# Performance work log

Hardware: AMD Instinct MI355X
Metric: run time of the kernel (lower is better)

## Reference

```python
import jax, jax.numpy as jnp
import numpy as np

N = 100000       # num nodes
E = 1000000      # num edges
D_IN = 128       # input feature dim
D_H = 64         # hidden = output dim
EPS = 1e-5       # GraphNorm eps
SLOPE = 0.2      # LeakyReLU negative slope


def _glorot(key, shape):
    lim = float(np.sqrt(6.0 / (shape[0] + shape[1])))
    return jax.random.uniform(key, shape, jnp.float32, -lim, lim)


def setup_inputs() -> dict:
    key = jax.random.key(0)
    ks = jax.random.split(key, 6)
    return {
        "x": jax.random.normal(ks[0], (N, D_IN), jnp.float32),
        "edge_index": jax.random.randint(ks[1], (2, E), 0, N),
        "W_in": _glorot(ks[2], (D_IN, D_H)),
        "b_in": jnp.zeros((D_H,), jnp.float32),
        "W1": _glorot(ks[3], (D_H, D_H)),
        "b1": jnp.zeros((D_H,), jnp.float32),
        "gn1_alpha": jnp.ones((D_H,), jnp.float32),
        "gn1_gamma": jnp.ones((D_H,), jnp.float32),
        "gn1_beta": jnp.zeros((D_H,), jnp.float32),
        "W2": _glorot(ks[4], (D_H, D_H)),
        "b2": jnp.zeros((D_H,), jnp.float32),
        "gn2_alpha": jnp.ones((D_H,), jnp.float32),
        "gn2_gamma": jnp.ones((D_H,), jnp.float32),
        "gn2_beta": jnp.zeros((D_H,), jnp.float32),
    }


def gcn_conv(x, W, b, src, dst):
    # GCNConv with added self-loops and symmetric normalization:
    # out = D^{-1/2} (A + I) D^{-1/2} (x W) + b
    xw = x @ W                                                 # [N, D]
    ones = jnp.ones((src.shape[0],), x.dtype)
    deg = jax.ops.segment_sum(ones, dst, num_segments=x.shape[0]) + 1.0  # +1 self-loop
    dinv = jax.lax.rsqrt(deg)                                  # [N]
    coef = dinv[src] * dinv[dst]                               # [E]
    agg = jax.ops.segment_sum(xw[src] * coef[:, None], dst, num_segments=x.shape[0])
    return agg + xw * (dinv * dinv)[:, None] + b


def graph_norm(x, alpha, gamma, beta):
    # PyG GraphNorm over a single graph: per-feature mean/var over all nodes
    mean = jnp.mean(x, axis=0)
    c = x - alpha * mean
    var = jnp.mean(c * c, axis=0)
    return gamma * c * jax.lax.rsqrt(var + EPS) + beta


def reference(x, edge_index, W_in, b_in, W1, b1, gn1_alpha, gn1_gamma, gn1_beta,
              W2, b2, gn2_alpha, gn2_gamma, gn2_beta):
    src, dst = edge_index[0], edge_index[1]
    h = x @ W_in + b_in                                        # input projection
    h = graph_norm(gcn_conv(h, W1, b1, src, dst), gn1_alpha, gn1_gamma, gn1_beta)
    h = jnp.where(h > 0, h, SLOPE * h)                         # LeakyReLU(0.2); dropout=eval (identity)
    h = graph_norm(gcn_conv(h, W2, b2, src, dst), gn2_alpha, gn2_gamma, gn2_beta)
    return h                                                    # [N, D_H]
```

## Files before the change

kernel.cpp:

```cpp
#include <hip/hip_runtime.h>
#include <stdint.h>

#define N_NODES 100000
#define N_EDGES 1000000
#define D_IN 128
#define D_H 64
#define EPS 1e-5f
#define SLOPE 0.2f

typedef unsigned short u16;
typedef unsigned int u32;
typedef __attribute__((ext_vector_type(8))) short bf16x8;
typedef __attribute__((ext_vector_type(4))) float f32x4;

#define SLAB_U16 ((size_t)(N_NODES + 1) * 16)
#define SLAB_D32 ((size_t)(N_NODES + 1) * 8)

__device__ __forceinline__ float bf2f(u16 u) {
    union { u32 i; float f; } v; v.i = ((u32)u) << 16; return v.f;
}
__device__ __forceinline__ u16 f2bf(float f) {
    union { float f; u32 i; } v; v.f = f;
    u32 r = (v.i + 0x7fffu + ((v.i >> 16) & 1u)) >> 16;
    return (u16)r;
}
__device__ __forceinline__ bool is_f32(const void* flagp) {
    return *(const u32*)flagp == 0x3F800000u;
}
__device__ __forceinline__ float loadf(const void* p, size_t i, bool m) {
    return m ? ((const float*)p)[i] : bf2f(((const u16*)p)[i]);
}

__global__ void kprep(const void* __restrict__ W_in, const void* __restrict__ b_in,
                      const void* __restrict__ W1, const void* __restrict__ W2,
                      const void* __restrict__ flagp,
                      u16* __restrict__ WcT, u16* __restrict__ W2T,
                      float* __restrict__ bc, u16* __restrict__ xwb_pad)
{
    bool m = is_f32(flagp);
    int t = threadIdx.x;
    if (blockIdx.x < 64) {
        int c = blockIdx.x;
        __shared__ float w1c[D_H];
        if (t < D_H) w1c[t] = loadf(W1, t * D_H + c, m);
        __syncthreads();
        float acc = 0.f;
        #pragma unroll 8
        for (int j = 0; j < D_H; j++) acc += loadf(W_in, t * D_H + j, m) * w1c[j];
        WcT[c * D_IN + t] = f2bf(acc);
        if (t == 0) {
            float b = 0.f;
            for (int j = 0; j < D_H; j++) b += loadf(b_in, j, m) * w1c[j];
            bc[c] = b;
        }
        if (c == 0 && t < D_H) {
            int s = t >> 4, w = t & 15;
            xwb_pad[(size_t)s * SLAB_U16 + (size_t)N_NODES * 16 + w] = 0;
        }
    } else {
        int idx = (blockIdx.x - 64) * 128 + t;
        int n = idx >> 6, k = idx & 63;
        W2T[n * D_H + k] = f2bf(loadf(W2, k * D_H + n, m));
    }
}

__global__ void kfill(const int* __restrict__ ei, int* __restrict__ cnt,
                      int* __restrict__ bucket)
{
    int e = blockIdx.x * blockDim.x + threadIdx.x;
    if (e >= N_EDGES) return;
    int s = ei[e];
    int d = ei[N_EDGES + e];
    int slot = atomicAdd(&cnt[d], 1);
    if (slot < 64) bucket[(size_t)d * 64 + slot] = s;
}

__global__ __launch_bounds__(256) void kgemm1(const void* __restrict__ x,
        const u16* __restrict__ WcT, const float* __restrict__ bc,
        const int* __restrict__ cnt, const void* __restrict__ flagp,
        u16* __restrict__ xwb)
{
    bool m = is_f32(flagp);
    __shared__ __align__(16) u16 xs[64 * 136];
    __shared__ __align__(16) u16 WT[64 * 136];
    int tid = threadIdx.x;
    int row0 = blockIdx.x * 64;
    for (int i = tid; i < 64 * 32; i += 256) {
        int r = i >> 5, kq = (i & 31) * 4;
        *(ushort4*)(WT + r * 136 + kq) = *(const ushort4*)(WcT + r * D_IN + kq);
    }
    for (int i = tid; i < 64 * 32; i += 256) {
        int r = i >> 5, kq = (i & 31) * 4;
        int gr = row0 + r;
        ushort4 u = make_ushort4(0, 0, 0, 0);
        if (gr < N_NODES) {
            if (m) {
                float4 v = *(const float4*)((const float*)x + (size_t)gr * D_IN + kq);
                u = make_ushort4(f2bf(v.x), f2bf(v.y), f2bf(v.z), f2bf(v.w));
            } else {
                u = *(const ushort4*)((const u16*)x + (size_t)gr * D_IN + kq);
            }
        }
        *(ushort4*)(xs + r * 136 + kq) = u;
    }
    __syncthreads();
    int w = tid >> 6, L = tid & 63;
    int q = L >> 4, c = L & 15;
    f32x4 acc[4];
    #pragma unroll
    for (int ct = 0; ct < 4; ct++) {
        float b = bc[ct * 16 + c];
        acc[ct] = (f32x4){b, b, b, b};
    }
    const u16* ap = xs + (w * 16 + c) * 136 + q * 8;
    #pragma unroll
    for (int kk = 0; kk < 4; kk++) {
        bf16x8 af = *(const bf16x8*)(ap + kk * 32);
        #pragma unroll
        for (int ct = 0; ct < 4; ct++) {
            bf16x8 bfr = *(const bf16x8*)(WT + (ct * 16 + c) * 136 + kk * 32 + q * 8);
            acc[ct] = __builtin_amdgcn_mfma_f32_16x16x32_bf16(af, bfr, acc[ct], 0, 0, 0);
        }
    }
    #pragma unroll
    for (int r = 0; r < 4; r++) {
        int gr = row0 + w * 16 + q * 4 + r;
        if (gr < N_NODES) {
            float ds = rsqrtf((float)cnt[gr] + 1.0f);
            #pragma unroll
            for (int ct = 0; ct < 4; ct++)
                xwb[(size_t)ct * SLAB_U16 + (size_t)gr * 16 + c] = f2bf(acc[ct][r] * ds);
        }
    }
}

__global__ __launch_bounds__(256) void kagg(const u16* __restrict__ xwb,
        const int* __restrict__ cnt, const int* __restrict__ bucket,
        const void* __restrict__ bvec, const void* __restrict__ flagp,
        u16* __restrict__ ybuf, float* __restrict__ accum)
{
    bool m = is_f32(flagp);
    __shared__ float red_s[4][64], red_q[4][64];
    int tid = threadIdx.x;
    int wv = tid >> 6, L = tid & 63;
    int r = L >> 3, c = L & 7;
    int node0 = blockIdx.x * 32 + wv * 8;

    int cnt8 = cnt[node0 + (L & 7)];
    int tl = L >> 4, sl = L & 15;
    int raw0 = bucket[(size_t)(node0 + tl) * 64 + sl];
    int raw1 = bucket[(size_t)(node0 + 4 + tl) * 64 + sl];

    int sv[16];
    #pragma unroll
    for (int n = 0; n < 8; n++) {
        int dgn = min(__shfl(cnt8, n), 64);
        int ngl = node0 + n;
        #pragma unroll
        for (int g = 0; g < 2; g++) {
            int slot = g * 8 + r;
            int rw = __shfl((n < 4) ? raw0 : raw1, (n & 3) * 16 + slot);
            sv[n * 2 + g] = slot < dgn ? rw : (slot == dgn ? ngl : N_NODES);
        }
    }

    int cvr = __shfl(cnt8, r);
    int dgr = min(cvr, 64);
    int nr = node0 + r;
    float dd = rsqrtf((float)cvr + 1.0f);
    bool anyrem = __any(dgr >= 16);

    #pragma unroll
    for (int p = 0; p < 4; p++) {
        const u32* slab = (const u32*)xwb + (size_t)p * SLAB_D32;
        u32 q[16];
        #pragma unroll
        for (int i = 0; i < 16; i++) q[i] = slab[(size_t)sv[i] * 8 + c];

        float fA0 = 0.f, fA1 = 0.f;
        #pragma unroll
        for (int n = 0; n < 8; n++) {
            u32 a = q[n * 2], b = q[n * 2 + 1];
            float f0 = __uint_as_float(a << 16) + __uint_as_float(b << 16);
            float f1 = __uint_as_float(a & 0xffff0000u) + __uint_as_float(b & 0xffff0000u);
            f0 += __shfl_xor(f0, 8);  f1 += __shfl_xor(f1, 8);
            f0 += __shfl_xor(f0, 16); f1 += __shfl_xor(f1, 16);
            f0 += __shfl_xor(f0, 32); f1 += __shfl_xor(f1, 32);
            if (r == n) { fA0 = f0; fA1 = f1; }
        }

        if (anyrem) {
            for (int s = 16; s <= 64; s++) {
                if (!__any(s <= dgr)) break;
                if (s <= dgr) {
                    int sv2 = (s < dgr) ? bucket[(size_t)nr * 64 + s] : nr;
                    u32 v = slab[(size_t)sv2 * 8 + c];
                    fA0 += __uint_as_float(v << 16);
                    fA1 += __uint_as_float(v & 0xffff0000u);
                }
            }
        }

        float b0 = loadf(bvec, p * 16 + 2 * c, m);
        float b1 = loadf(bvec, p * 16 + 2 * c + 1, m);
        float y0 = dd * fA0 + b0;
        float y1 = dd * fA1 + b1;
        ((u32*)ybuf)[(size_t)p * SLAB_D32 + (size_t)nr * 8 + c] =
            (u32)f2bf(y0) | ((u32)f2bf(y1) << 16);

        float s0 = y0, s1 = y1, q0 = y0 * y0, q1 = y1 * y1;
        s0 += __shfl_xor(s0, 8);  s1 += __shfl_xor(s1, 8);
        q0 += __shfl_xor(q0, 8);  q1 += __shfl_xor(q1, 8);
        s0 += __shfl_xor(s0, 16); s1 += __shfl_xor(s1, 16);
        q0 += __shfl_xor(q0, 16); q1 += __shfl_xor(q1, 16);
        s0 += __shfl_xor(s0, 32); s1 += __shfl_xor(s1, 32);
        q0 += __shfl_xor(q0, 32); q1 += __shfl_xor(q1, 32);
        if (r == 0) {
            red_s[wv][p * 16 + 2 * c] = s0;  red_s[wv][p * 16 + 2 * c + 1] = s1;
            red_q[wv][p * 16 + 2 * c] = q0;  red_q[wv][p * 16 + 2 * c + 1] = q1;
        }
    }

    __syncthreads();
    if (tid < 64) {
        atomicAdd(&accum[tid],      red_s[0][tid] + red_s[1][tid] + red_s[2][tid] + red_s[3][tid]);
        atomicAdd(&accum[64 + tid], red_q[0][tid] + red_q[1][tid] + red_q[2][tid] + red_q[3][tid]);
    }
}

__global__ __launch_bounds__(256) void kgemm2(const u16* __restrict__ y1b,
        const u16* __restrict__ W2T, const float* __restrict__ accum,
        const void* __restrict__ alpha, const void* __restrict__ gamma,
        const void* __restrict__ beta, const void* __restrict__ flagp,
        const int* __restrict__ cnt, u16* __restrict__ xwb)
{
    bool m = is_f32(flagp);
    __shared__ __align__(16) u16 hs[64 * 72];
    __shared__ __align__(16) u16 WT[64 * 72];
    __shared__ float aL[64], cL[64];
    int tid = threadIdx.x;
    if (tid < 64) {
        float mean = accum[tid] * (1.0f / N_NODES);
        float al = loadf(alpha, tid, m);
        float var = accum[64 + tid] * (1.0f / N_NODES) - mean * mean * al * (2.0f - al);
        var = fmaxf(var, 0.f);
        float a = loadf(gamma, tid, m) * rsqrtf(var + EPS);
        aL[tid] = a;
        cL[tid] = loadf(beta, tid, m) - a * al * mean;
    }
    for (int i = tid; i < 64 * 16; i += 256) {
        int r = i >> 4, kq = (i & 15) * 4;
        *(ushort4*)(WT + r * 72 + kq) = *(const ushort4*)(W2T + r * D_H + kq);
    }
    __syncthreads();
    int row0 = blockIdx.x * 64;
    for (int i = tid; i < 64 * 16; i += 256) {
        int r = i >> 4, kq = (i & 15) * 4;
        int gr = row0 + r;
        ushort4 u = make_ushort4(0, 0, 0, 0);
        if (gr < N_NODES) {
            int s = kq >> 4, off = kq & 15;
            u = *(const ushort4*)(y1b + (size_t)s * SLAB_U16 + (size_t)gr * 16 + off);
        }
        float h0 = aL[kq + 0] * bf2f(u.x) + cL[kq + 0]; h0 = h0 > 0.f ? h0 : SLOPE * h0;
        float h1 = aL[kq + 1] * bf2f(u.y) + cL[kq + 1]; h1 = h1 > 0.f ? h1 : SLOPE * h1;
        float h2 = aL[kq + 2] * bf2f(u.z) + cL[kq + 2]; h2 = h2 > 0.f ? h2 : SLOPE * h2;
        float h3 = aL[kq + 3] * bf2f(u.w) + cL[kq + 3]; h3 = h3 > 0.f ? h3 : SLOPE * h3;
        *(ushort4*)(hs + r * 72 + kq) = make_ushort4(f2bf(h0), f2bf(h1), f2bf(h2), f2bf(h3));
    }
    __syncthreads();
    int w = tid >> 6, L = tid & 63;
    int q = L >> 4, c = L & 15;
    f32x4 acc[4] = {};
    const u16* ap = hs + (w * 16 + c) * 72 + q * 8;
    #pragma unroll
    for (int kk = 0; kk < 2; kk++) {
        bf16x8 af = *(const bf16x8*)(ap + kk * 32);
        #pragma unroll
        for (int ct = 0; ct < 4; ct++) {
            bf16x8 bfr = *(const bf16x8*)(WT + (ct * 16 + c) * 72 + kk * 32 + q * 8);
            acc[ct] = __builtin_amdgcn_mfma_f32_16x16x32_bf16(af, bfr, acc[ct], 0, 0, 0);
        }
    }
    #pragma unroll
    for (int r = 0; r < 4; r++) {
        int gr = row0 + w * 16 + q * 4 + r;
        if (gr < N_NODES) {
            float ds = rsqrtf((float)cnt[gr] + 1.0f);
            #pragma unroll
            for (int ct = 0; ct < 4; ct++)
                xwb[(size_t)ct * SLAB_U16 + (size_t)gr * 16 + c] = f2bf(acc[ct][r] * ds);
        }
    }
}

__global__ __launch_bounds__(256) void kout(const u16* __restrict__ y2b,
        const float* __restrict__ accum2, const void* __restrict__ alpha,
        const void* __restrict__ gamma, const void* __restrict__ beta,
        const void* __restrict__ flagp, void* __restrict__ out)
{
    bool m = is_f32(flagp);
    __shared__ float a2[64], c2[64];
    int tid = threadIdx.x;
    if (tid < 64) {
        float mean = accum2[tid] * (1.0f / N_NODES);
        float al = loadf(alpha, tid, m);
        float var = accum2[64 + tid] * (1.0f / N_NODES) - mean * mean * al * (2.0f - al);
        var = fmaxf(var, 0.f);
        float a = loadf(gamma, tid, m) * rsqrtf(var + EPS);
        a2[tid] = a;
        c2[tid] = loadf(beta, tid, m) - a * al * mean;
    }
    __syncthreads();
    int gid = blockIdx.x * 256 + tid;
    int nd = gid >> 4, q4 = gid & 15;
    int s = q4 >> 2, pr = q4 & 3;
    const u32* yp = (const u32*)y2b + (size_t)s * SLAB_D32 + (size_t)nd * 8 + pr * 2;
    u32 v0 = yp[0];
    u32 v1 = yp[1];
    int f = q4 * 4;
    float o0 = a2[f + 0] * __uint_as_float(v0 << 16)          + c2[f + 0];
    float o1 = a2[f + 1] * __uint_as_float(v0 & 0xffff0000u)  + c2[f + 1];
    float o2 = a2[f + 2] * __uint_as_float(v1 << 16)          + c2[f + 2];
    float o3 = a2[f + 3] * __uint_as_float(v1 & 0xffff0000u)  + c2[f + 3];
    if (m) {
        *(float4*)((float*)out + (size_t)nd * 64 + f) = make_float4(o0, o1, o2, o3);
    } else {
        u32 p0 = (u32)f2bf(o0) | ((u32)f2bf(o1) << 16);
        u32 p1 = (u32)f2bf(o2) | ((u32)f2bf(o3) << 16);
        *(uint2*)((u32*)out + (size_t)nd * 32 + f / 2) = make_uint2(p0, p1);
    }
}

extern "C" void kernel_launch(void* const* d_in, const int* in_sizes, int n_in,
                              void* d_out, int out_size, void* d_ws, size_t ws_size,
                              hipStream_t stream)
{
    const void* x    = d_in[0];
    const int*  ei   = (const int*)d_in[1];
    const void* W_in = d_in[2];
    const void* b_in = d_in[3];
    const void* W1   = d_in[4];
    const void* b1   = d_in[5];
    const void* gn1a = d_in[6];
    const void* gn1g = d_in[7];
    const void* gn1b = d_in[8];
    const void* W2   = d_in[9];
    const void* b2   = d_in[10];
    const void* gn2a = d_in[11];
    const void* gn2g = d_in[12];
    const void* gn2b = d_in[13];

    char* ws = (char*)d_ws;
    int*   cnt    = (int*)(ws + 0);
    float* accum  = (float*)(ws + 400000);
    float* bc     = (float*)(ws + 402048);
    u16*   WcT    = (u16*)(ws + 402432);
    u16*   W2T    = (u16*)(ws + 418816);
    int*   bucket = (int*)(ws + 1235200);
    u16*   bufA   = (u16*)(ws + 26835200);
    u16*   bufB   = (u16*)(ws + 39635456);

    hipMemsetAsync(ws, 0, 400000 + 1024, stream);

    kprep<<<96, 128, 0, stream>>>(W_in, b_in, W1, W2, gn1a, WcT, W2T, bc, bufA);
    kfill<<<(N_EDGES + 255) / 256, 256, 0, stream>>>(ei, cnt, bucket);
    kgemm1<<<(N_NODES + 63) / 64, 256, 0, stream>>>(x, WcT, bc, cnt, gn1a, bufA);
    kagg<<<N_NODES / 32, 256, 0, stream>>>(bufA, cnt, bucket, b1, gn1a, bufB, accum);
    kgemm2<<<(N_NODES + 63) / 64, 256, 0, stream>>>(bufB, W2T, accum, gn1a, gn1g, gn1b, gn1a, cnt, bufA);
    kagg<<<N_NODES / 32, 256, 0, stream>>>(bufA, cnt, bucket, b2, gn1a, bufB, accum + 128);
    kout<<<N_NODES * 16 / 256, 256, 0, stream>>>(bufB, accum + 128, gn2a, gn2g, gn2b, gn1a, d_out);
}
```

Baseline: 413.8 us.

## Split aggregation into per-slab passes and fuse weight prep with edge bucketing

The aggregation kernel is split into four launches, one per 16-feature slab. Each pass gathers only a 3.2 MB slab, so the random neighbor gathers can hit in L2/MALL instead of streaming across all slabs in one kernel. The weight-prep and edge-bucket fill kernels are merged into one launch, and bucket writes use nontemporal stores. The cost is re-reading the bucket and count arrays and recomputing indices in every pass, plus more kernel launches.

```diff
diff --git a/kernel.cpp b/kernel.cpp
--- a/kernel.cpp
+++ b/kernel.cpp
@@ -31,23 +31,28 @@
     return m ? ((const float*)p)[i] : bf2f(((const u16*)p)[i]);
 }
 
-__global__ void kprep(const void* __restrict__ W_in, const void* __restrict__ b_in,
-                      const void* __restrict__ W1, const void* __restrict__ W2,
-                      const void* __restrict__ flagp,
-                      u16* __restrict__ WcT, u16* __restrict__ W2T,
-                      float* __restrict__ bc, u16* __restrict__ xwb_pad)
+__global__ __launch_bounds__(256) void kpf(const void* __restrict__ W_in,
+                     const void* __restrict__ b_in,
+                     const void* __restrict__ W1, const void* __restrict__ W2,
+                     const void* __restrict__ flagp, const int* __restrict__ ei,
+                     u16* __restrict__ WcT, u16* __restrict__ W2T,
+                     float* __restrict__ bc, u16* __restrict__ xwb_pad,
+                     int* __restrict__ cnt, int* __restrict__ bucket)
 {
     bool m = is_f32(flagp);
     int t = threadIdx.x;
-    if (blockIdx.x < 64) {
-        int c = blockIdx.x;
+    int bid = blockIdx.x;
+    if (bid < 64) {
+        int c = bid;
         __shared__ float w1c[D_H];
         if (t < D_H) w1c[t] = loadf(W1, t * D_H + c, m);
         __syncthreads();
-        float acc = 0.f;
-        #pragma unroll 8
-        for (int j = 0; j < D_H; j++) acc += loadf(W_in, t * D_H + j, m) * w1c[j];
-        WcT[c * D_IN + t] = f2bf(acc);
+        if (t < D_IN) {
+            float acc = 0.f;
+            #pragma unroll 8
+            for (int j = 0; j < D_H; j++) acc += loadf(W_in, t * D_H + j, m) * w1c[j];
+            WcT[c * D_IN + t] = f2bf(acc);
+        }
         if (t == 0) {
             float b = 0.f;
             for (int j = 0; j < D_H; j++) b += loadf(b_in, j, m) * w1c[j];
@@ -57,22 +62,20 @@
             int s = t >> 4, w = t & 15;
             xwb_pad[(size_t)s * SLAB_U16 + (size_t)N_NODES * 16 + w] = 0;
         }
-    } else {
-        int idx = (blockIdx.x - 64) * 128 + t;
+    } else if (bid < 80) {
+        int idx = (bid - 64) * 256 + t;
         int n = idx >> 6, k = idx & 63;
         W2T[n * D_H + k] = f2bf(loadf(W2, k * D_H + n, m));
-    }
-}
-
-__global__ void kfill(const int* __restrict__ ei, int* __restrict__ cnt,
-                      int* __restrict__ bucket)
-{
-    int e = blockIdx.x * blockDim.x + threadIdx.x;
-    if (e >= N_EDGES) return;
-    int s = ei[e];
-    int d = ei[N_EDGES + e];
-    int slot = atomicAdd(&cnt[d], 1);
-    if (slot < 64) bucket[(size_t)d * 64 + slot] = s;
+    } else {
+        int e = (bid - 80) * 256 + t;
+        if (e < N_EDGES) {
+            int s = ei[e];
+            int d = ei[N_EDGES + e];
+            int slot = atomicAdd(&cnt[d], 1);
+            if (slot < 64)
+                __builtin_nontemporal_store(s, &bucket[(size_t)d * 64 + slot]);
+        }
+    }
 }
 
 __global__ __launch_bounds__(256) void kgemm1(const void* __restrict__ x,
@@ -134,13 +137,13 @@
     }
 }
 
-__global__ __launch_bounds__(256) void kagg(const u16* __restrict__ xwb,
+__global__ __launch_bounds__(256) void kagg_pass(const u16* __restrict__ xwb,
         const int* __restrict__ cnt, const int* __restrict__ bucket,
         const void* __restrict__ bvec, const void* __restrict__ flagp,
-        u16* __restrict__ ybuf, float* __restrict__ accum)
-{
-    bool m = is_f32(flagp);
-    __shared__ float red_s[4][64], red_q[4][64];
+        u16* __restrict__ ybuf, float* __restrict__ accum, int pass)
+{
+    bool m = is_f32(flagp);
+    __shared__ float red_s[4][16], red_q[4][16];
     int tid = threadIdx.x;
     int wv = tid >> 6, L = tid & 63;
     int r = L >> 3, c = L & 7;
@@ -170,61 +173,59 @@
     float dd = rsqrtf((float)cvr + 1.0f);
     bool anyrem = __any(dgr >= 16);
 
-    #pragma unroll
-    for (int p = 0; p < 4; p++) {
-        const u32* slab = (const u32*)xwb + (size_t)p * SLAB_D32;
-        u32 q[16];
-        #pragma unroll
-        for (int i = 0; i < 16; i++) q[i] = slab[(size_t)sv[i] * 8 + c];
-
-        float fA0 = 0.f, fA1 = 0.f;
-        #pragma unroll
-        for (int n = 0; n < 8; n++) {
-            u32 a = q[n * 2], b = q[n * 2 + 1];
-            float f0 = __uint_as_float(a << 16) + __uint_as_float(b << 16);
-            float f1 = __uint_as_float(a & 0xffff0000u) + __uint_as_float(b & 0xffff0000u);
-            f0 += __shfl_xor(f0, 8);  f1 += __shfl_xor(f1, 8);
-            f0 += __shfl_xor(f0, 16); f1 += __shfl_xor(f1, 16);
-            f0 += __shfl_xor(f0, 32); f1 += __shfl_xor(f1, 32);
-            if (r == n) { fA0 = f0; fA1 = f1; }
-        }
-
-        if (anyrem) {
-            for (int s = 16; s <= 64; s++) {
-                if (!__any(s <= dgr)) break;
-                if (s <= dgr) {
-                    int sv2 = (s < dgr) ? bucket[(size_t)nr * 64 + s] : nr;
-                    u32 v = slab[(size_t)sv2 * 8 + c];
-                    fA0 += __uint_as_float(v << 16);
-                    fA1 += __uint_as_float(v & 0xffff0000u);
-                }
+    const u32* slab = (const u32*)xwb + (size_t)pass * SLAB_D32;
+    u32 q[16];
+    #pragma unroll
+    for (int i = 0; i < 16; i++) q[i] = slab[(size_t)sv[i] * 8 + c];
+
+    float fA0 = 0.f, fA1 = 0.f;
+    #pragma unroll
+    for (int n = 0; n < 8; n++) {
+        u32 a = q[n * 2], b = q[n * 2 + 1];
+        float f0 = __uint_as_float(a << 16) + __uint_as_float(b << 16);
+        float f1 = __uint_as_float(a & 0xffff0000u) + __uint_as_float(b & 0xffff0000u);
+        f0 += __shfl_xor(f0, 8);  f1 += __shfl_xor(f1, 8);
+        f0 += __shfl_xor(f0, 16); f1 += __shfl_xor(f1, 16);
+        f0 += __shfl_xor(f0, 32); f1 += __shfl_xor(f1, 32);
+        if (r == n) { fA0 = f0; fA1 = f1; }
+    }
+
+    if (anyrem) {
+        for (int s = 16; s <= 64; s++) {
+            if (!__any(s <= dgr)) break;
+            if (s <= dgr) {
+                int sv2 = (s < dgr) ? bucket[(size_t)nr * 64 + s] : nr;
+                u32 v = slab[(size_t)sv2 * 8 + c];
+                fA0 += __uint_as_float(v << 16);
+                fA1 += __uint_as_float(v & 0xffff0000u);
             }
         }
-
-        float b0 = loadf(bvec, p * 16 + 2 * c, m);
-        float b1 = loadf(bvec, p * 16 + 2 * c + 1, m);
-        float y0 = dd * fA0 + b0;
-        float y1 = dd * fA1 + b1;
-        ((u32*)ybuf)[(size_t)p * SLAB_D32 + (size_t)nr * 8 + c] =
-            (u32)f2bf(y0) | ((u32)f2bf(y1) << 16);
-
-        float s0 = y0, s1 = y1, q0 = y0 * y0, q1 = y1 * y1;
-        s0 += __shfl_xor(s0, 8);  s1 += __shfl_xor(s1, 8);
-        q0 += __shfl_xor(q0, 8);  q1 += __shfl_xor(q1, 8);
-        s0 += __shfl_xor(s0, 16); s1 += __shfl_xor(s1, 16);
-        q0 += __shfl_xor(q0, 16); q1 += __shfl_xor(q1, 16);
-        s0 += __shfl_xor(s0, 32); s1 += __shfl_xor(s1, 32);
-        q0 += __shfl_xor(q0, 32); q1 += __shfl_xor(q1, 32);
-        if (r == 0) {
-            red_s[wv][p * 16 + 2 * c] = s0;  red_s[wv][p * 16 + 2 * c + 1] = s1;
-            red_q[wv][p * 16 + 2 * c] = q0;  red_q[wv][p * 16 + 2 * c + 1] = q1;
-        }
-    }
-
-    __syncthreads();
-    if (tid < 64) {
-        atomicAdd(&accum[tid],      red_s[0][tid] + red_s[1][tid] + red_s[2][tid] + red_s[3][tid]);
-        atomicAdd(&accum[64 + tid], red_q[0][tid] + red_q[1][tid] + red_q[2][tid] + red_q[3][tid]);
+    }
+
+    float b0 = loadf(bvec, pass * 16 + 2 * c, m);
+    float b1 = loadf(bvec, pass * 16 + 2 * c + 1, m);
+    float y0 = dd * fA0 + b0;
+    float y1 = dd * fA1 + b1;
+    ((u32*)ybuf)[(size_t)pass * SLAB_D32 + (size_t)nr * 8 + c] =
+        (u32)f2bf(y0) | ((u32)f2bf(y1) << 16);
+
+    float s0 = y0, s1 = y1, q0 = y0 * y0, q1 = y1 * y1;
+    s0 += __shfl_xor(s0, 8);  s1 += __shfl_xor(s1, 8);
+    q0 += __shfl_xor(q0, 8);  q1 += __shfl_xor(q1, 8);
+    s0 += __shfl_xor(s0, 16); s1 += __shfl_xor(s1, 16);
+    q0 += __shfl_xor(q0, 16); q1 += __shfl_xor(q1, 16);
+    s0 += __shfl_xor(s0, 32); s1 += __shfl_xor(s1, 32);
+    q0 += __shfl_xor(q0, 32); q1 += __shfl_xor(q1, 32);
+    if (r == 0) {
+        red_s[wv][2 * c] = s0;  red_s[wv][2 * c + 1] = s1;
+        red_q[wv][2 * c] = q0;  red_q[wv][2 * c + 1] = q1;
+    }
+    __syncthreads();
+    if (tid < 16) {
+        atomicAdd(&accum[pass * 16 + tid],
+                  red_s[0][tid] + red_s[1][tid] + red_s[2][tid] + red_s[3][tid]);
+        atomicAdd(&accum[64 + pass * 16 + tid],
+                  red_q[0][tid] + red_q[1][tid] + red_q[2][tid] + red_q[3][tid]);
     }
 }
 
@@ -363,11 +364,17 @@
 
     hipMemsetAsync(ws, 0, 400000 + 1024, stream);
 
-    kprep<<<96, 128, 0, stream>>>(W_in, b_in, W1, W2, gn1a, WcT, W2T, bc, bufA);
-    kfill<<<(N_EDGES + 255) / 256, 256, 0, stream>>>(ei, cnt, bucket);
+    kpf<<<80 + (N_EDGES + 255) / 256, 256, 0, stream>>>(
+        W_in, b_in, W1, W2, gn1a, ei, WcT, W2T, bc, bufA, cnt, bucket);
     kgemm1<<<(N_NODES + 63) / 64, 256, 0, stream>>>(x, WcT, bc, cnt, gn1a, bufA);
-    kagg<<<N_NODES / 32, 256, 0, stream>>>(bufA, cnt, bucket, b1, gn1a, bufB, accum);
-    kgemm2<<<(N_NODES + 63) / 64, 256, 0, stream>>>(bufB, W2T, accum, gn1a, gn1g, gn1b, gn1a, cnt, bufA);
-    kagg<<<N_NODES / 32, 256, 0, stream>>>(bufA, cnt, bucket, b2, gn1a, bufB, accum + 128);
-    kout<<<N_NODES * 16 / 256, 256, 0, stream>>>(bufB, accum + 128, gn2a, gn2g, gn2b, gn1a, d_out);
-}
+    for (int p = 0; p < 4; p++)
+        kagg_pass<<<N_NODES / 32, 256, 0, stream>>>(bufA, cnt, bucket, b1, gn1a,
+                                                    bufB, accum, p);
+    kgemm2<<<(N_NODES + 63) / 64, 256, 0, stream>>>(bufB, W2T, accum, gn1a, gn1g,
+                                                    gn1b, gn1a, cnt, bufA);
+    for (int p = 0; p < 4; p++)
+        kagg_pass<<<N_NODES / 32, 256, 0, stream>>>(bufA, cnt, bucket, b2, gn1a,
+                                                    bufB, accum + 128, p);
+    kout<<<N_NODES * 16 / 256, 256, 0, stream>>>(bufB, accum + 128, gn2a, gn2g,
+                                                 gn2b, gn1a, d_out);
+}
```

New measurement: 602.8 us. 1.46x slower.
